# Kernel tuning notes

Hardware: AMD Instinct MI355X
Metric: run time of the kernel (lower is better)

## Reference

```python
import jax, jax.numpy as jnp
import numpy as np

H = 16  # number of heads

def setup_inputs() -> dict:
    key = jax.random.key(0)
    ks = jax.random.split(key, 9)
    B, N, D = 2, 2048, 1024
    s = 0.02
    q = jax.random.normal(ks[0], (B, N, D), jnp.float32)
    k = jax.random.normal(ks[1], (B, N, D), jnp.float32)
    v = jax.random.normal(ks[2], (B, N, D), jnp.float32)
    mask = jax.random.randint(ks[3], (B, 1, N, N), 0, 2).astype(bool)
    Wq = jax.random.normal(ks[4], (D, D), jnp.float32) * s
    Wk = jax.random.normal(ks[5], (D, D), jnp.float32) * s
    Wv = jax.random.normal(ks[6], (D, D), jnp.float32) * s
    Wo = jax.random.normal(ks[7], (D, D), jnp.float32) * s
    bq = jnp.zeros((D,), jnp.float32)
    bk = jnp.zeros((D,), jnp.float32)
    bv = jnp.zeros((D,), jnp.float32)
    bo = jnp.zeros((D,), jnp.float32)
    return {"q": q, "k": k, "v": v, "mask": mask,
            "Wq": Wq, "bq": bq, "Wk": Wk, "bk": bk,
            "Wv": Wv, "bv": bv, "Wo": Wo, "bo": bo}


def reference(q, k, v, mask, Wq, bq, Wk, bk, Wv, bv, Wo, bo):
    B, N, D = q.shape
    dk = D // H
    # nn.Linear: x @ W.T + b, then split heads: b n (h d) -> b h n d
    def proj(x, W, b):
        return (x @ W.T + b).reshape(B, N, H, dk).transpose(0, 2, 1, 3)
    qh = proj(q, Wq, bq)  # [B,H,N,dk]
    kh = proj(k, Wk, bk)
    vh = proj(v, Wv, bv)
    # NOTE: original has NO 1/sqrt(dk) scaling
    score = jnp.einsum('bhnd,bhmd->bhnm', qh, kh)
    score = jnp.where(mask, jnp.float32(-1e9), score)
    attn = jax.nn.softmax(score, axis=-1)
    x = jnp.einsum('bhnm,bhmd->bhnd', attn, vh)
    x = x.transpose(0, 2, 1, 3).reshape(B, N, D)  # b h n d -> b n (h d)
    return x @ Wo.T + bo
```

## Files before the change

### kernel.cpp

```cpp
#include <hip/hip_runtime.h>
#include <math.h>

#define BB 2
#define NN 2048
#define DD 1024
#define HH 16
#define DK 64
#define LOG2E 1.4426950408889634f

typedef __attribute__((ext_vector_type(8))) short short8;
typedef __attribute__((ext_vector_type(4))) float f32x4;
typedef __attribute__((ext_vector_type(16))) float f32x16;
typedef __attribute__((ext_vector_type(4))) float f32x4v;
typedef __attribute__((ext_vector_type(8))) unsigned short ushort8;
typedef __attribute__((ext_vector_type(4))) unsigned short ushort4v;
typedef unsigned long long u64;

__device__ __forceinline__ unsigned short f2bf(float f) {
  unsigned u = __float_as_uint(f);
  unsigned r = (u + 0x7FFFu + ((u >> 16) & 1u)) >> 16;
  return (unsigned short)r;
}

__device__ __forceinline__ unsigned cvtpk(float a, float b) {
  unsigned r;
  asm("v_cvt_pk_bf16_f32 %0, %1, %2" : "=v"(r) : "v"(a), "v"(b));
  return r;
}

__device__ __forceinline__ void gload_lds16(const void* g, void* l) {
  auto gp = (const __attribute__((address_space(1))) unsigned int*)(unsigned long long)g;
  auto lp = (__attribute__((address_space(3))) unsigned int*)(unsigned int)(unsigned long long)l;
  __builtin_amdgcn_global_load_lds(gp, lp, 16, 0, 0);
}

__global__ __launch_bounds__(256) void cvt_all(
    const float* __restrict__ q, const float* __restrict__ k, const float* __restrict__ v,
    const float* __restrict__ wq, const float* __restrict__ wk, const float* __restrict__ wv,
    const float* __restrict__ wo, unsigned short* __restrict__ ws)
{
  const long NW = (long)DD * DD;
  const long NX = (long)BB * NN * DD;
  long i = ((long)blockIdx.x * blockDim.x + threadIdx.x) * 8;
  if (i >= 4 * NW + 3 * NX) return;
  const float* src; unsigned short* dst; long off;
  if (i < 4 * NW) {
    int s = (int)(i / NW);
    src = (s == 0) ? wq : (s == 1) ? wk : (s == 2) ? wv : wo;
    off = i - (long)s * NW;
    dst = ws + (long)s * NW + off;
  } else {
    long j = i - 4 * NW;
    int s = (int)(j / NX);
    src = (s == 0) ? q : (s == 1) ? k : v;
    off = j - (long)s * NX;
    dst = ws + 4 * NW + (long)s * NX + off;
  }
  f32x4v a = *(const f32x4v*)(src + off);
  f32x4v b = *(const f32x4v*)(src + off + 4);
  ushort8 o;
  o[0] = f2bf(a[0]); o[1] = f2bf(a[1]); o[2] = f2bf(a[2]); o[3] = f2bf(a[3]);
  o[4] = f2bf(b[0]); o[5] = f2bf(b[1]); o[6] = f2bf(b[2]); o[7] = f2bf(b[3]);
  *(ushort8*)dst = o;
}

__global__ __launch_bounds__(256) void cvt_mask_bits(const void* __restrict__ mask,
                                                     u64* __restrict__ mb, long total64)
{
  const unsigned char* m8 = (const unsigned char*)mask;
  const int l = threadIdx.x & 63;
  unsigned probe = m8[l * 4 + 1] | m8[l * 4 + 2] | m8[l * 4 + 3];
  const bool isBool = (__any(probe != 0) != 0);

  long t = (long)blockIdx.x * blockDim.x + threadIdx.x;
  if (t >= total64) return;
  u64 bits = 0;
  if (isBool) {
    const uint4* p = (const uint4*)(m8 + t * 64);
#pragma unroll
    for (int i = 0; i < 4; ++i) {
      uint4 q4 = p[i];
      unsigned vv[4] = {q4.x, q4.y, q4.z, q4.w};
#pragma unroll
      for (int j = 0; j < 4; ++j)
#pragma unroll
        for (int bb = 0; bb < 4; ++bb)
          bits |= (u64)((vv[j] >> (8 * bb)) & 1u) << (i * 16 + j * 4 + bb);
    }
  } else {
    const int4* p = (const int4*)((const int*)mask + t * 64);
#pragma unroll
    for (int i = 0; i < 16; ++i) {
      int4 q4 = p[i];
      bits |= (u64)(q4.x & 1) << (i * 4);
      bits |= (u64)(q4.y & 1) << (i * 4 + 1);
      bits |= (u64)(q4.z & 1) << (i * 4 + 2);
      bits |= (u64)(q4.w & 1) << (i * 4 + 3);
    }
  }
  const long bb2 = t >> 16;
  const long qq = (t >> 5) & 2047;
  const long tcol = t & 31;
  mb[(bb2 * 32 + tcol) * 2048 + qq] = bits;
}

struct GemmArgs {
  const unsigned short* A;
  const unsigned short* Bw;
  const float* bias;
  void* C;
  int mode;
  float oscale;
};

template<int TM, int BN>
__global__ __launch_bounds__(256) void gemm_bt(GemmArgs ga0, GemmArgs ga1, GemmArgs ga2)
{
  constexpr int K = DD;
  constexpr int Nn = DD;
  constexpr int GX = 1024 / BN;
  constexpr int GY = 4096 / TM;
  constexpr int PERZ = GX * GY;
  constexpr int MF = TM / 32;
  constexpr int NF = BN / 32;
  constexpr int NT = K / 32;
  constexpr int LPS = TM / 64 + BN / 64;
  __shared__ __align__(16) unsigned short As[3][TM * 32];
  __shared__ __align__(16) unsigned short Bs[3][BN * 32];

  int wgid = blockIdx.x + (blockIdx.y + blockIdx.z * GY) * GX;
  const int nwg = (int)gridDim.z * PERZ;
  const int chunk = nwg >> 3;
  wgid = (wgid & 7) * chunk + (wgid >> 3);
  const int zi = wgid / PERZ;
  const int rem = wgid % PERZ;
  const int m0 = (rem / GX) * TM;
  const int n0 = (rem % GX) * BN;
  GemmArgs ga = (zi == 0) ? ga0 : ((zi == 1) ? ga1 : ga2);

  const int tid = threadIdx.x;
  const int lane = tid & 63;
  const int w = tid >> 6;
  const int m_woff = (w >> 1) * (TM / 2);
  const int n_woff = (w & 1) * (BN / 2);
  const int c = lane & 15, g = lane >> 4;

  f32x4 acc[MF][NF];
  const f32x4 z4 = {0.f, 0.f, 0.f, 0.f};
#pragma unroll
  for (int m = 0; m < MF; ++m)
#pragma unroll
    for (int n = 0; n < NF; ++n) acc[m][n] = z4;

  const unsigned short* Ab = ga.A + (long)m0 * K;
  const unsigned short* Bb = ga.Bw + (long)n0 * K;
  const int ar = tid >> 2;
  const int ac = ((tid & 3) ^ (ar & 3)) * 8;

  auto STAGE = [&](int buf, int kk) {
#pragma unroll
    for (int i = 0; i < TM / 64; ++i)
      gload_lds16(Ab + (long)(i * 64 + ar) * K + kk + ac, &As[buf][i * 2048 + tid * 8]);
#pragma unroll
    for (int i = 0; i < BN / 64; ++i)
      gload_lds16(Bb + (long)(i * 64 + ar) * K + kk + ac, &Bs[buf][i * 2048 + tid * 8]);
  };

  STAGE(0, 0);
  STAGE(1, 32);

  const int rswz = (g ^ (c & 3)) * 8;

  for (int t = 0; t < NT; ++t) {
    if (t < NT - 1) {
      if constexpr (LPS == 4)
        asm volatile("s_waitcnt vmcnt(4)" ::: "memory");
      else
        asm volatile("s_waitcnt vmcnt(3)" ::: "memory");
    } else {
      asm volatile("s_waitcnt vmcnt(0)" ::: "memory");
    }
    __builtin_amdgcn_s_barrier();
    __builtin_amdgcn_sched_barrier(0);
    if (t + 2 < NT) STAGE((t + 2) % 3, (t + 2) * 32);

    const int cb = t % 3;
    short8 a[MF], b[NF];
#pragma unroll
    for (int m = 0; m < MF; ++m)
      a[m] = *(const short8*)&As[cb][(m_woff + 16 * m + c) * 32 + rswz];
#pragma unroll
    for (int n = 0; n < NF; ++n)
      b[n] = *(const short8*)&Bs[cb][(n_woff + 16 * n + c) * 32 + rswz];
    __builtin_amdgcn_s_setprio(1);
#pragma unroll
    for (int m = 0; m < MF; ++m)
#pragma unroll
      for (int n = 0; n < NF; ++n)
        acc[m][n] = __builtin_amdgcn_mfma_f32_16x16x32_bf16(a[m], b[n], acc[m][n], 0, 0, 0);
    __builtin_amdgcn_s_setprio(0);
  }

#pragma unroll
  for (int n = 0; n < NF; ++n) {
    const int col = n0 + n_woff + 16 * n + c;
    const float bv = ga.bias[col];
#pragma unroll
    for (int m = 0; m < MF; ++m) {
      const int row0 = m0 + m_woff + 16 * m + 4 * g;
      if (ga.mode == 2) {
        ushort4v pk;
#pragma unroll
        for (int r = 0; r < 4; ++r) pk[r] = f2bf((acc[m][n][r] + bv) * ga.oscale);
        *(ushort4v*)&((unsigned short*)ga.C)[((long)(row0 >> 11) * DD + col) * NN + (row0 & (NN - 1))] = pk;
      } else {
#pragma unroll
        for (int r = 0; r < 4; ++r) {
          const int row = row0 + r;
          const float val = (acc[m][n][r] + bv) * ga.oscale;
          if (ga.mode == 1)
            ((float*)ga.C)[(long)row * Nn + col] = val;
          else
            ((unsigned short*)ga.C)[(long)row * Nn + col] = f2bf(val);
        }
      }
    }
  }
}

__global__ __launch_bounds__(512) void attn_kernel(
    const unsigned short* __restrict__ Q,
    const unsigned short* __restrict__ K,
    const unsigned short* __restrict__ Vt,
    const u64* __restrict__ mb64,
    unsigned short* __restrict__ ctx)
{
  __shared__ __align__(16) char lds_raw[65536];
  unsigned short* KsB = (unsigned short*)lds_raw;
  unsigned short* VsB = (unsigned short*)(lds_raw + 32768);
  float* OB = (float*)lds_raw;

  const int tid = threadIdx.x;
  const int lane = tid & 63;
  const int w = tid >> 6;
  const int grp = w >> 2;
  const int wq = w & 3;
  const int bid = blockIdx.x;
  const int b = (bid >> 4) & 1, h = bid & 15;
  const int q0 = (bid >> 5) * 128;
  const int l31 = lane & 31;
  const int hi = lane >> 5;
  const int qrow = q0 + 32 * wq + l31;

  short8 aq[4];
  {
    const unsigned short* qp = Q + ((long)(b * NN + qrow)) * DD + h * DK + 8 * hi;
    aq[0] = *(const short8*)(qp);
    aq[1] = *(const short8*)(qp + 16);
    aq[2] = *(const short8*)(qp + 32);
    aq[3] = *(const short8*)(qp + 48);
  }

  f32x16 o0, o1, cinit;
#pragma unroll
  for (int r = 0; r < 16; ++r) { o0[r] = 0.f; o1[r] = 0.f; cinit[r] = -28.853901f; }
  float ls0 = 0.f, ls1 = 0.f;

  const unsigned short* Kbase = K + (long)(b * NN) * DD + h * DK;
  const unsigned short* Vbase = Vt + ((long)(b * DD + h * DK)) * NN;
  const u64* mbase = mb64 + (long)(b * 32) * 2048 + qrow;

  const int srow = tid >> 3;
  const int scol = tid & 7;
  const int swcol = scol ^ (srow & 7);

  auto STAGE = [&](int buf, int t) {
    gload_lds16(Kbase + (long)(t * 64 + srow) * DD + swcol * 8, &KsB[buf * 4096 + tid * 8]);
    gload_lds16(Vbase + (long)srow * NN + t * 64 + swcol * 8, &VsB[buf * 4096 + tid * 8]);
    gload_lds16(Kbase + (long)((t + 16) * 64 + srow) * DD + swcol * 8, &KsB[(2 + buf) * 4096 + tid * 8]);
    gload_lds16(Vbase + (long)srow * NN + (t + 16) * 64 + swcol * 8, &VsB[(2 + buf) * 4096 + tid * 8]);
  };

  int koffs[8], voff0[4], voff1[4];
#pragma unroll
  for (int sub = 0; sub < 2; ++sub) {
    const int krow = l31 + 32 * sub;
    const int kswz = (l31 & 7) << 3;
#pragma unroll
    for (int i = 0; i < 4; ++i)
      koffs[sub * 4 + i] = krow * 64 + ((16 * i + 8 * hi) ^ kswz);
#pragma unroll
    for (int dblk = 0; dblk < 2; ++dblk) {
      const int vrow = l31 + 32 * dblk;
      voff0[sub * 2 + dblk] = vrow * 64 + ((32 * sub + 8 * hi) ^ kswz);
      voff1[sub * 2 + dblk] = vrow * 64 + ((32 * sub + 16 + 8 * hi) ^ kswz);
    }
  }

  STAGE(0, 0);
  __syncthreads();
  int cur = 0;
  const int sh4 = 4 * hi;
  u64 mword = mbase[(long)(grp * 16) * 2048];

  for (int t = 0; t < 16; ++t) {
    const int tt = grp * 16 + t;
    const u64 mnext = (t < 15) ? mbase[(long)(tt + 1) * 2048] : 0;
    if (t < 15) STAGE(cur ^ 1, t + 1);
    const unsigned msk0 = ((unsigned)mword) >> sh4;
    const unsigned msk1 = ((unsigned)(mword >> 32)) >> sh4;
    const unsigned short* Kt = &KsB[(grp * 2 + cur) * 4096];
    const unsigned short* Vtl = &VsB[(grp * 2 + cur) * 4096];

#pragma unroll
    for (int sub = 0; sub < 2; ++sub) {
      const unsigned m = sub ? msk1 : msk0;

      f32x16 ss = cinit;
      __builtin_amdgcn_s_setprio(1);
#pragma unroll
      for (int i = 0; i < 4; ++i) {
        const short8 kf = *(const short8*)&Kt[koffs[sub * 4 + i]];
        ss = __builtin_amdgcn_mfma_f32_32x32x16_bf16(kf, aq[i], ss, 0, 0, 0);
      }
      __builtin_amdgcn_s_setprio(0);

      unsigned wv[8];
      float lacc = 0.f;
#pragma unroll
      for (int i = 0; i < 8; ++i) {
        const int r0 = 2 * i, r1 = 2 * i + 1;
        const int cr0 = (r0 & 3) + 8 * (r0 >> 2);
        const int cr1 = (r1 & 3) + 8 * (r1 >> 2);
        const float e0 = ((m >> cr0) & 1u) ? -1e9f : ss[r0];
        const float e1 = ((m >> cr1) & 1u) ? -1e9f : ss[r1];
        const float p0 = __builtin_amdgcn_exp2f(e0);
        const float p1 = __builtin_amdgcn_exp2f(e1);
        lacc += p0 + p1;
        wv[i] = cvtpk(p0, p1);
      }
      if (sub == 0) ls0 += lacc; else ls1 += lacc;

      asm("v_permlane32_swap_b32 %0, %1" : "+v"(wv[0]), "+v"(wv[2]));
      asm("v_permlane32_swap_b32 %0, %1" : "+v"(wv[1]), "+v"(wv[3]));
      asm("v_permlane32_swap_b32 %0, %1" : "+v"(wv[4]), "+v"(wv[6]));
      asm("v_permlane32_swap_b32 %0, %1" : "+v"(wv[5]), "+v"(wv[7]));
      union { short8 s; unsigned u[4]; } pa0, pa1;
      pa0.u[0] = wv[0]; pa0.u[1] = wv[1]; pa0.u[2] = wv[2]; pa0.u[3] = wv[3];
      pa1.u[0] = wv[4]; pa1.u[1] = wv[5]; pa1.u[2] = wv[6]; pa1.u[3] = wv[7];

      __builtin_amdgcn_s_setprio(1);
      {
        const short8 vb00 = *(const short8*)&Vtl[voff0[sub * 2 + 0]];
        const short8 vb10 = *(const short8*)&Vtl[voff1[sub * 2 + 0]];
        o0 = __builtin_amdgcn_mfma_f32_32x32x16_bf16(pa0.s, vb00, o0, 0, 0, 0);
        o0 = __builtin_amdgcn_mfma_f32_32x32x16_bf16(pa1.s, vb10, o0, 0, 0, 0);
        const short8 vb01 = *(const short8*)&Vtl[voff0[sub * 2 + 1]];
        const short8 vb11 = *(const short8*)&Vtl[voff1[sub * 2 + 1]];
        o1 = __builtin_amdgcn_mfma_f32_32x32x16_bf16(pa0.s, vb01, o1, 0, 0, 0);
        o1 = __builtin_amdgcn_mfma_f32_32x32x16_bf16(pa1.s, vb11, o1, 0, 0, 0);
      }
      __builtin_amdgcn_s_setprio(0);
    }
    __syncthreads();
    cur ^= 1;
    mword = mnext;
  }

  float lsum = ls0 + ls1;
  const int li = wq * 64 + lane;
  if (grp == 1) {
    float* dst = OB + (long)li * 33;
#pragma unroll
    for (int r = 0; r < 16; ++r) { dst[r] = o0[r]; dst[16 + r] = o1[r]; }
    dst[32] = lsum;
  }
  __syncthreads();
  if (grp == 0) {
    const float* src = OB + (long)li * 33;
#pragma unroll
    for (int r = 0; r < 16; ++r) { o0[r] += src[r]; o1[r] += src[16 + r]; }
    lsum += src[32];
    lsum += __shfl_xor(lsum, 32);
    const float inv = 1.0f / lsum;

#pragma unroll
    for (int r = 0; r < 16; ++r) {
      const int qr = (r & 3) + 8 * (r >> 2) + 4 * hi;
      const float linv = __shfl(inv, qr);
      const long row = (long)(b * NN + q0 + 32 * wq + qr);
      ctx[row * DD + h * DK + l31] = f2bf(o0[r] * linv);
      ctx[row * DD + h * DK + 32 + l31] = f2bf(o1[r] * linv);
    }
  }
}

extern "C" void kernel_launch(void* const* d_in, const int* in_sizes, int n_in,
                              void* d_out, int out_size, void* d_ws, size_t ws_size,
                              hipStream_t stream) {
  const float* q  = (const float*)d_in[0];
  const float* k  = (const float*)d_in[1];
  const float* v  = (const float*)d_in[2];
  const void*  mask = d_in[3];
  const float* Wq = (const float*)d_in[4];
  const float* bq = (const float*)d_in[5];
  const float* Wk = (const float*)d_in[6];
  const float* bk = (const float*)d_in[7];
  const float* Wv = (const float*)d_in[8];
  const float* bv = (const float*)d_in[9];
  const float* Wo = (const float*)d_in[10];
  const float* bo = (const float*)d_in[11];

  unsigned short* ws = (unsigned short*)d_ws;
  const long NW = (long)DD * DD;
  const long NX = (long)BB * NN * DD;
  unsigned short* Wqb = ws;
  unsigned short* Wkb = ws + NW;
  unsigned short* Wvb = ws + 2 * NW;
  unsigned short* Wob = ws + 3 * NW;
  unsigned short* Xq  = ws + 4 * NW;
  unsigned short* Xk  = Xq + NX;
  unsigned short* Xv  = Xk + NX;
  unsigned short* Qh  = Xv + NX;
  unsigned short* Kh  = Qh + NX;
  unsigned short* Vtr = Kh + NX;
  unsigned short* Ctx = Vtr + NX;
  u64* Mbits = (u64*)(Ctx + NX);
  const long NM64 = (long)BB * NN * NN / 64;

  cvt_all<<<8192, 256, 0, stream>>>(q, k, v, Wq, Wk, Wv, Wo, ws);
  cvt_mask_bits<<<(int)(NM64 / 256), 256, 0, stream>>>(mask, Mbits, NM64);

  GemmArgs gq = {Xq, Wqb, bq, (void*)Qh, 0, LOG2E};
  GemmArgs gk = {Xk, Wkb, bk, (void*)Kh, 0, 1.0f};
  GemmArgs gv = {Xv, Wvb, bv, (void*)Vtr, 2, 1.0f};
  dim3 gproj(DD / 128, (BB * NN) / 128, 3);
  gemm_bt<128, 128><<<gproj, 256, 0, stream>>>(gq, gk, gv);

  attn_kernel<<<512, 512, 0, stream>>>(Qh, Kh, Vtr, Mbits, Ctx);

  GemmArgs go = {Ctx, Wob, bo, d_out, 1, 1.0f};
  dim3 gout(DD / 128, (BB * NN) / 64, 1);
  gemm_bt<64, 128><<<gout, 256, 0, stream>>>(go, go, go);
}
```

Before: 130.1 us.

## Drop split-KV wave groups and use a triple-buffered async K/V pipeline

The attention kernel used to run 8 waves split into two KV-half groups, each double-buffered, and merged the partial outputs through LDS at the end. It now runs 4 waves that each walk all 32 KV tiles, using a 3-slot LDS ring with manual vmcnt waits and one barrier per tile. The goal is to keep two tiles in flight, drop the cross-group reduction, and cut LDS use to 48KB so more blocks fit per CU. In exchange each block does twice the serial KV iterations with half the waves, which lowers per-block parallelism, and the hand-written waitcnt counts must match the number of issued loads.

```diff
diff --git a/kernel.cpp b/kernel.cpp
--- a/kernel.cpp
+++ b/kernel.cpp
@@ -228,29 +228,25 @@
   }
 }
 
-__global__ __launch_bounds__(512) void attn_kernel(
+__global__ __launch_bounds__(256) void attn_kernel(
     const unsigned short* __restrict__ Q,
     const unsigned short* __restrict__ K,
     const unsigned short* __restrict__ Vt,
     const u64* __restrict__ mb64,
     unsigned short* __restrict__ ctx)
 {
-  __shared__ __align__(16) char lds_raw[65536];
-  unsigned short* KsB = (unsigned short*)lds_raw;
-  unsigned short* VsB = (unsigned short*)(lds_raw + 32768);
-  float* OB = (float*)lds_raw;
+  __shared__ __align__(16) unsigned short Ks[3][64 * 64];
+  __shared__ __align__(16) unsigned short Vs[3][64 * 64];
 
   const int tid = threadIdx.x;
   const int lane = tid & 63;
   const int w = tid >> 6;
-  const int grp = w >> 2;
-  const int wq = w & 3;
   const int bid = blockIdx.x;
   const int b = (bid >> 4) & 1, h = bid & 15;
   const int q0 = (bid >> 5) * 128;
   const int l31 = lane & 31;
   const int hi = lane >> 5;
-  const int qrow = q0 + 32 * wq + l31;
+  const int qrow = q0 + 32 * w + l31;
 
   short8 aq[4];
   {
@@ -275,10 +271,12 @@
   const int swcol = scol ^ (srow & 7);
 
   auto STAGE = [&](int buf, int t) {
-    gload_lds16(Kbase + (long)(t * 64 + srow) * DD + swcol * 8, &KsB[buf * 4096 + tid * 8]);
-    gload_lds16(Vbase + (long)srow * NN + t * 64 + swcol * 8, &VsB[buf * 4096 + tid * 8]);
-    gload_lds16(Kbase + (long)((t + 16) * 64 + srow) * DD + swcol * 8, &KsB[(2 + buf) * 4096 + tid * 8]);
-    gload_lds16(Vbase + (long)srow * NN + (t + 16) * 64 + swcol * 8, &VsB[(2 + buf) * 4096 + tid * 8]);
+#pragma unroll
+    for (int hf = 0; hf < 2; ++hf) {
+      const int row = srow + 32 * hf;
+      gload_lds16(Kbase + (long)(t * 64 + row) * DD + swcol * 8, &Ks[buf][hf * 2048 + tid * 8]);
+      gload_lds16(Vbase + (long)row * NN + t * 64 + swcol * 8, &Vs[buf][hf * 2048 + tid * 8]);
+    }
   };
 
   int koffs[8], voff0[4], voff1[4];
@@ -297,21 +295,11 @@
     }
   }
 
-  STAGE(0, 0);
-  __syncthreads();
-  int cur = 0;
   const int sh4 = 4 * hi;
-  u64 mword = mbase[(long)(grp * 16) * 2048];
-
-  for (int t = 0; t < 16; ++t) {
-    const int tt = grp * 16 + t;
-    const u64 mnext = (t < 15) ? mbase[(long)(tt + 1) * 2048] : 0;
-    if (t < 15) STAGE(cur ^ 1, t + 1);
-    const unsigned msk0 = ((unsigned)mword) >> sh4;
-    const unsigned msk1 = ((unsigned)(mword >> 32)) >> sh4;
-    const unsigned short* Kt = &KsB[(grp * 2 + cur) * 4096];
-    const unsigned short* Vtl = &VsB[(grp * 2 + cur) * 4096];
-
+
+  auto COMPUTE = [&](int cb, unsigned msk0, unsigned msk1) {
+    const unsigned short* Kt = &Ks[cb][0];
+    const unsigned short* Vtl = &Vs[cb][0];
 #pragma unroll
     for (int sub = 0; sub < 2; ++sub) {
       const unsigned m = sub ? msk1 : msk0;
@@ -362,36 +350,53 @@
       }
       __builtin_amdgcn_s_setprio(0);
     }
-    __syncthreads();
-    cur ^= 1;
-    mword = mnext;
+  };
+
+  STAGE(0, 0);
+  u64 mwA = mbase[0];
+  STAGE(1, 1);
+  u64 mwB = mbase[2048];
+
+#pragma unroll 1
+  for (int t = 0; t < 32; t += 2) {
+    asm volatile("s_waitcnt vmcnt(5)" ::: "memory");
+    __builtin_amdgcn_s_barrier();
+    __builtin_amdgcn_sched_barrier(0);
+    {
+      const unsigned msk0 = ((unsigned)mwA) >> sh4;
+      const unsigned msk1 = ((unsigned)(mwA >> 32)) >> sh4;
+      if (t + 2 < 32) {
+        STAGE((t + 2) % 3, t + 2);
+        mwA = mbase[(long)(t + 2) * 2048];
+      }
+      COMPUTE(t % 3, msk0, msk1);
+    }
+    if (t + 1 < 31) asm volatile("s_waitcnt vmcnt(5)" ::: "memory");
+    else            asm volatile("s_waitcnt vmcnt(0)" ::: "memory");
+    __builtin_amdgcn_s_barrier();
+    __builtin_amdgcn_sched_barrier(0);
+    {
+      const unsigned msk0 = ((unsigned)mwB) >> sh4;
+      const unsigned msk1 = ((unsigned)(mwB >> 32)) >> sh4;
+      if (t + 3 < 32) {
+        STAGE((t + 3) % 3, t + 3);
+        mwB = mbase[(long)(t + 3) * 2048];
+      }
+      COMPUTE((t + 1) % 3, msk0, msk1);
+    }
   }
 
   float lsum = ls0 + ls1;
-  const int li = wq * 64 + lane;
-  if (grp == 1) {
-    float* dst = OB + (long)li * 33;
-#pragma unroll
-    for (int r = 0; r < 16; ++r) { dst[r] = o0[r]; dst[16 + r] = o1[r]; }
-    dst[32] = lsum;
-  }
-  __syncthreads();
-  if (grp == 0) {
-    const float* src = OB + (long)li * 33;
-#pragma unroll
-    for (int r = 0; r < 16; ++r) { o0[r] += src[r]; o1[r] += src[16 + r]; }
-    lsum += src[32];
-    lsum += __shfl_xor(lsum, 32);
-    const float inv = 1.0f / lsum;
-
-#pragma unroll
-    for (int r = 0; r < 16; ++r) {
-      const int qr = (r & 3) + 8 * (r >> 2) + 4 * hi;
-      const float linv = __shfl(inv, qr);
-      const long row = (long)(b * NN + q0 + 32 * wq + qr);
-      ctx[row * DD + h * DK + l31] = f2bf(o0[r] * linv);
-      ctx[row * DD + h * DK + 32 + l31] = f2bf(o1[r] * linv);
-    }
+  lsum += __shfl_xor(lsum, 32);
+  const float inv = 1.0f / lsum;
+
+#pragma unroll
+  for (int r = 0; r < 16; ++r) {
+    const int qr = (r & 3) + 8 * (r >> 2) + 4 * hi;
+    const float linv = __shfl(inv, qr);
+    const long row = (long)(b * NN + q0 + 32 * w + qr);
+    ctx[row * DD + h * DK + l31] = f2bf(o0[r] * linv);
+    ctx[row * DD + h * DK + 32 + l31] = f2bf(o1[r] * linv);
   }
 }
 
@@ -437,7 +442,7 @@
   dim3 gproj(DD / 128, (BB * NN) / 128, 3);
   gemm_bt<128, 128><<<gproj, 256, 0, stream>>>(gq, gk, gv);
 
-  attn_kernel<<<512, 512, 0, stream>>>(Qh, Kh, Vtr, Mbits, Ctx);
+  attn_kernel<<<512, 256, 0, stream>>>(Qh, Kh, Vtr, Mbits, Ctx);
 
   GemmArgs go = {Ctx, Wob, bo, d_out, 1, 1.0f};
   dim3 gout(DD / 128, (BB * NN) / 64, 1);
```

Measured after the change: 136.4 us. +4.9%, slower.
